# Kernel tuning notes

Hardware: AMD Instinct MI355X
Metric: run time of the kernel (lower is better)

## Reference

```python
import jax, jax.numpy as jnp
import numpy as np

B = 4
N_PER_B = 65536
N = B * N_PER_B
GROUP_SIZE = 64
ORDER = 9  # min bits to cover grid size 512
C0, C1, C2 = 64, 128, 128


def hilbert_encode(coors, order):
    """Skilling AxesToTranspose, vectorized over N points, 3 dims -> int32 code."""
    n = 3
    X = [coors[:, i].astype(jnp.int32) for i in range(n)]
    M = 1 << (order - 1)
    Q = M
    while Q > 1:
        P = Q - 1
        for i in range(n):
            cond = (X[i] & Q) != 0
            if i == 0:
                X[0] = jnp.where(cond, X[0] ^ P, X[0])
            else:
                t = (X[0] ^ X[i]) & P
                x0 = jnp.where(cond, X[0] ^ P, X[0] ^ t)
                xi = jnp.where(cond, X[i], X[i] ^ t)
                X[0], X[i] = x0, xi
        Q >>= 1
    for i in range(1, n):
        X[i] = X[i] ^ X[i - 1]
    t = jnp.zeros_like(X[0])
    Q = M
    while Q > 1:
        t = jnp.where((X[n - 1] & Q) != 0, t ^ (Q - 1), t)
        Q >>= 1
    X = [x ^ t for x in X]
    # interleave transposed bits MSB-first: code has 3*order bits (27 < 31, fits int32)
    code = jnp.zeros_like(X[0])
    for b in range(order - 1, -1, -1):
        for i in range(n):
            code = (code << 1) | ((X[i] >> b) & 1)
    return code


def _mapping_indices(vox_coors):
    """Two Hilbert orderings (normal + reversed coord axes); per-batch stable grouping."""
    batch = vox_coors[:, 0]
    c1 = vox_coors[:, 1:4]
    c2 = vox_coors[:, 3:0:-1]  # [0,3,2,1] reverse of the xyz columns
    code1 = hilbert_encode(c1, ORDER)
    code2 = hilbert_encode(c2, ORDER)
    ind1 = jnp.lexsort((code1, batch))  # batch-major, curve-order minor
    ind2 = jnp.lexsort((code2, batch))
    inv1 = jnp.argsort(ind1)
    ind12 = inv1[ind2]  # maps ordering-1 arrangement to ordering-2 arrangement
    return ind1, ind12


def _block(p, x, params):
    """VoxFormer-style block: center pts per group, pos-encode, gate feats, local attn, FFN."""
    Wpos, bpos, Wq, Wk, Wv, Wo, Wout = params
    C = Wq.shape[0]
    gs = GROUP_SIZE
    pg = p.reshape(-1, gs, 3)
    e = (pg - pg.mean(axis=1, keepdims=True)).reshape(-1, 3) @ Wpos + bpos  # [N,C]
    h = (x * e).reshape(-1, gs, C)  # [G,gs,C]
    q, k, v = h @ Wq, h @ Wk, h @ Wv
    scores = jnp.einsum('gqc,gkc->gqk', q, k) / jnp.sqrt(jnp.asarray(C, q.dtype))
    attn = jax.nn.softmax(scores, axis=-1)
    o = jnp.einsum('gqk,gkc->gqc', attn, v).reshape(-1, C) @ Wo
    return jax.nn.relu(o) @ Wout  # [N,C_out]


def setup_inputs() -> dict:
    key = jax.random.key(0)
    ks = jax.random.split(key, 20)
    bcol = jnp.repeat(jnp.arange(B, dtype=jnp.int32), N_PER_B)
    z = jax.random.randint(ks[0], (N,), 0, 64, dtype=jnp.int32)
    y = jax.random.randint(ks[1], (N,), 0, 512, dtype=jnp.int32)
    x = jax.random.randint(ks[2], (N,), 0, 512, dtype=jnp.int32)
    vox_coors = jnp.stack([bcol, z, y, x], axis=1)
    vox_numbs = jnp.full((B,), N_PER_B, dtype=jnp.int32)
    vox_feats = jax.random.normal(ks[3], (N, C0), dtype=jnp.float32)
    pts_coors = jax.random.normal(ks[4], (N, 3), dtype=jnp.float32)
    s = lambda k, shape: jax.random.normal(k, shape, dtype=jnp.float32) / np.float32(np.sqrt(shape[0]))
    return dict(
        vox_numbs=vox_numbs, vox_coors=vox_coors, vox_feats=vox_feats, pts_coors=pts_coors,
        Wpos1=s(ks[5], (3, C0)), bpos1=jnp.zeros((C0,), jnp.float32),
        Wq1=s(ks[6], (C0, C0)), Wk1=s(ks[7], (C0, C0)), Wv1=s(ks[8], (C0, C0)),
        Wo1=s(ks[9], (C0, C0)), Wout1=s(ks[10], (C0, C1)),
        Wpos2=s(ks[11], (3, C1)), bpos2=jnp.zeros((C1,), jnp.float32),
        Wq2=s(ks[12], (C1, C1)), Wk2=s(ks[13], (C1, C1)), Wv2=s(ks[14], (C1, C1)),
        Wo2=s(ks[15], (C1, C1)), Wout2=s(ks[16], (C1, C2)),
    )


def reference(vox_numbs, vox_coors, vox_feats, pts_coors,
              Wpos1, bpos1, Wq1, Wk1, Wv1, Wo1, Wout1,
              Wpos2, bpos2, Wq2, Wk2, Wv2, Wo2, Wout2):
    ind1, ind12 = _mapping_indices(vox_coors)
    params = ((Wpos1, bpos1, Wq1, Wk1, Wv1, Wo1, Wout1),
              (Wpos2, bpos2, Wq2, Wk2, Wv2, Wo2, Wout2))
    for ind, prm in zip((ind1, ind12), params):
        vox_feats = vox_feats[ind]
        pts_coors = pts_coors[ind]
        vox_coors = vox_coors[ind]
        vox_feats = _block(pts_coors, vox_feats, prm)
    return vox_feats, pts_coors, vox_coors, vox_numbs
```

## Files before the change

kernel.cpp:

```cpp
#include <hip/hip_runtime.h>

using u64 = unsigned long long;
typedef _Float16 f16;
using f16x8 = __attribute__((ext_vector_type(8))) _Float16;
using f16x4 = __attribute__((ext_vector_type(4))) _Float16;
using f32x4 = __attribute__((ext_vector_type(4))) float;

__device__ __forceinline__ int hilbert3(int X0, int X1, int X2) {
  #pragma unroll
  for (int Q = 256; Q > 1; Q >>= 1) {
    const int P = Q - 1;
    if (X0 & Q) X0 ^= P;
    int t1 = (X0 ^ X1) & P;
    if (X1 & Q) X0 ^= P; else { X0 ^= t1; X1 ^= t1; }
    int t2 = (X0 ^ X2) & P;
    if (X2 & Q) X0 ^= P; else { X0 ^= t2; X2 ^= t2; }
  }
  X1 ^= X0;
  X2 ^= X1;
  int t = 0;
  #pragma unroll
  for (int Q = 256; Q > 1; Q >>= 1) if (X2 & Q) t ^= (Q - 1);
  X0 ^= t; X1 ^= t; X2 ^= t;
  int code = 0;
  #pragma unroll
  for (int b = 8; b >= 0; b--)
    code = (code << 3) | (((X0 >> b) & 1) << 2) | (((X1 >> b) & 1) << 1) | ((X2 >> b) & 1);
  return code;
}

__device__ __forceinline__ void cswap(u64& a, u64& b, bool up) {
  if ((a > b) == up) { u64 t = a; a = b; b = t; }
}

__global__ __launch_bounds__(1024) void sort_tile0(const int* __restrict__ vox,
                                                   u64* __restrict__ keys, int n,
                                                   int spanm1) {
  __shared__ u64 s[2048];
  const int base = blockIdx.x * 2048;
  const int bl = base & spanm1;
  #pragma unroll
  for (int m = 0; m < 2; m++) {
    const int e = base + threadIdx.x + m * 1024;
    const int isrc = e & (n - 1);
    const int4 c = ((const int4*)vox)[isrc];
    const unsigned code = (e < n) ? (unsigned)hilbert3(c.y, c.z, c.w)
                                  : (unsigned)hilbert3(c.w, c.z, c.y);
    s[threadIdx.x + m * 1024] =
        ((u64)(unsigned)c.x << 45) | ((u64)code << 18) | (unsigned)isrc;
  }
  __syncthreads();
  for (int k = 2; k <= 2048; k <<= 1) {
    for (int j = k >> 1; j >= 1; j >>= 1) {
      const int p = threadIdx.x;
      const int i = ((p & ~(j - 1)) << 1) | (p & (j - 1));
      const bool up = (((bl + i) & k) == 0);
      u64 a = s[i], b = s[i | j];
      if ((a > b) == up) { s[i] = b; s[i | j] = a; }
      __syncthreads();
    }
  }
  keys[base + threadIdx.x]        = s[threadIdx.x];
  keys[base + threadIdx.x + 1024] = s[threadIdx.x + 1024];
}

template<int LEV>
__device__ __forceinline__ void gstepT(u64* __restrict__ keys, int t, int jlow,
                                       int k, int spanm1) {
  constexpr int S = 1 << LEV;
  const int i0 = ((t & ~(jlow - 1)) << LEV) | (t & (jlow - 1));
  const bool up = (((i0 & spanm1) & k) == 0);
  u64 x[S];
  #pragma unroll
  for (int m = 0; m < S; m++) x[m] = keys[i0 + (size_t)m * jlow];
  #pragma unroll
  for (int d = S >> 1; d >= 1; d >>= 1)
    #pragma unroll
    for (int m = 0; m < S; m++)
      if (!(m & d)) cswap(x[m], x[m | d], up);
  #pragma unroll
  for (int m = 0; m < S; m++) keys[i0 + (size_t)m * jlow] = x[m];
}

__global__ void bitonic_gN(u64* __restrict__ keys, int jlow, int lev, int k, int spanm1) {
  const int t = blockIdx.x * blockDim.x + threadIdx.x;
  switch (lev) {
    case 1: gstepT<1>(keys, t, jlow, k, spanm1); break;
    case 2: gstepT<2>(keys, t, jlow, k, spanm1); break;
    case 3: gstepT<3>(keys, t, jlow, k, spanm1); break;
    default: gstepT<4>(keys, t, jlow, k, spanm1); break;
  }
}

__global__ __launch_bounds__(1024) void merge_tile2(u64* __restrict__ keys, int k,
                                                    int spanm1) {
  __shared__ u64 s[2048];
  const int base = blockIdx.x * 2048;
  s[threadIdx.x]        = keys[base + threadIdx.x];
  s[threadIdx.x + 1024] = keys[base + threadIdx.x + 1024];
  __syncthreads();
  const bool up = (((base & spanm1) & k) == 0);
  for (int j = 1024; j >= 1; j >>= 1) {
    const int p = threadIdx.x;
    const int i = ((p & ~(j - 1)) << 1) | (p & (j - 1));
    u64 a = s[i], b = s[i | j];
    if ((a > b) == up) { s[i] = b; s[i | j] = a; }
    __syncthreads();
  }
  keys[base + threadIdx.x]        = s[threadIdx.x];
  keys[base + threadIdx.x + 1024] = s[threadIdx.x + 1024];
}

__global__ void extract_inv_k(const u64* __restrict__ keys, const float* __restrict__ pts,
                              int* __restrict__ ind, int* __restrict__ inv,
                              float* __restrict__ pts1p, int n) {
  int t = blockIdx.x * blockDim.x + threadIdx.x;
  if (t >= n) return;
  int s = (int)(keys[t] & 0x3FFFFULL);
  ind[t] = s;
  inv[s] = t;
  pts1p[t * 3 + 0] = pts[s * 3 + 0];
  pts1p[t * 3 + 1] = pts[s * 3 + 1];
  pts1p[t * 3 + 2] = pts[s * 3 + 2];
}

__global__ void finish_k(const u64* __restrict__ keys2, const int* __restrict__ inv1,
                         int* __restrict__ g2, const float* __restrict__ pts,
                         const int* __restrict__ vox, const int* __restrict__ numbs,
                         float* __restrict__ out_pts, float* __restrict__ out_vox,
                         float* __restrict__ out_nb, int n, int B) {
  int t = blockIdx.x * blockDim.x + threadIdx.x;
  if (t >= n) return;
  int s = (int)(keys2[t] & 0x3FFFFULL);
  g2[t] = inv1[s];
  out_pts[t * 3 + 0] = pts[s * 3 + 0];
  out_pts[t * 3 + 1] = pts[s * 3 + 1];
  out_pts[t * 3 + 2] = pts[s * 3 + 2];
  const int4 v = ((const int4*)vox)[s];
  out_vox[t * 4 + 0] = (float)v.x;
  out_vox[t * 4 + 1] = (float)v.y;
  out_vox[t * 4 + 2] = (float)v.z;
  out_vox[t * 4 + 3] = (float)v.w;
  if (t < B) out_nb[t] = (float)numbs[t];
}

__global__ void prep_all(const float* __restrict__ Wq1, const float* __restrict__ Wk1,
                         const float* __restrict__ Wv1, const float* __restrict__ Wo1,
                         const float* __restrict__ Wout1,
                         const float* __restrict__ Wq2, const float* __restrict__ Wk2,
                         const float* __restrict__ Wv2, const float* __restrict__ Wo2,
                         const float* __restrict__ Wout2,
                         f16* __restrict__ A1a, f16* __restrict__ A2a, f16* __restrict__ A3a,
                         f16* __restrict__ A1b, f16* __restrict__ A2b, f16* __restrict__ A3b) {
  const int idx = blockIdx.x * blockDim.x + threadIdx.x;
  if (idx < 4096) {
    const int a = idx >> 6, b = idx & 63;
    float s1 = 0.f, s2 = 0.f;
    for (int c = 0; c < 64; c++) {
      s1 = fmaf(Wq1[b * 64 + c], Wk1[a * 64 + c], s1);
      s2 = fmaf(Wv1[b * 64 + c], Wo1[c * 64 + a], s2);
    }
    A1a[idx] = (f16)(s1 * 0.125f);
    A2a[idx] = (f16)s2;
  }
  if (idx < 8192) {
    const int o = idx >> 6, c = idx & 63;
    A3a[idx] = (f16)Wout1[c * 128 + o];
  }
  {
    const int a = idx >> 7, b = idx & 127;
    float s1 = 0.f, s2 = 0.f;
    for (int c = 0; c < 128; c++) {
      s1 = fmaf(Wq2[b * 128 + c], Wk2[a * 128 + c], s1);
      s2 = fmaf(Wv2[b * 128 + c], Wo2[c * 128 + a], s2);
    }
    A1b[idx] = (f16)(s1 * 0.08838834764831845f);
    A2b[idx] = (f16)s2;
    A3b[idx] = (f16)Wout2[b * 128 + a];
  }
}

__device__ __forceinline__ int swzb(int row) {
  return (((row & 7) ^ (((row >> 3) & 3) << 1)) << 4);
}

template<int M, int K, int AMODE>
__device__ __forceinline__ void stage8(const f16* __restrict__ Ag,
                                       const f16* __restrict__ lA,
                                       const f16* __restrict__ lB,
                                       int w, int lane,
                                       f32x4 (&acc)[(M / 16) * 4 / 8]) {
  constexpr int NPW = (M / 16) * 4 / 8;
  constexpr int KT = K / 32;
  const int lr = lane & 15, lk = lane >> 4;
  const int ct = (w * NPW) >> 2;
  const int qt0 = (w * NPW) & 3;
  const int c = ct * 16 + lr;
  f16x8 Af[KT];
  #pragma unroll
  for (int kt = 0; kt < KT; kt++) {
    const int k0 = kt * 32 + lk * 8;
    if (AMODE == 0) {
      Af[kt] = *(const f16x8*)(Ag + (size_t)c * K + k0);
    } else if (AMODE == 1) {
      Af[kt] = *(const f16x8*)((const char*)lA + (((c * K + k0) * 2) ^ swzb(c)));
    } else {
      f16x8 a;
      #pragma unroll
      for (int e = 0; e < 8; e++) {
        const int j = k0 + e;
        a[e] = *(const f16*)((const char*)lA + (((j * M + c) * 2) ^ swzb(j)));
      }
      Af[kt] = a;
    }
  }
  #pragma unroll
  for (int i = 0; i < NPW; i++) {
    const int q = lr + (qt0 + i) * 16;
    #pragma unroll
    for (int kt = 0; kt < KT; kt++) {
      const int k0 = kt * 32 + lk * 8;
      const f16x8 Bf = *(const f16x8*)((const char*)lB + (((q * K + k0) * 2) ^ swzb(q)));
      acc[i] = __builtin_amdgcn_mfma_f32_16x16x32_f16(Af[kt], Bf, acc[i], 0, 0, 0);
    }
  }
}

template<int RL, bool RELU>
__device__ __forceinline__ void store8(f16* __restrict__ dst, int ct, int qt,
                                       int lane, f32x4 v) {
  const int lr = lane & 15, lk = lane >> 4;
  const int q = lr + qt * 16;
  const int c0 = ct * 16 + lk * 4;
  f16x4 o;
  #pragma unroll
  for (int r = 0; r < 4; r++) {
    float x = v[r];
    if (RELU) x = fmaxf(x, 0.f);
    o[r] = (f16)x;
  }
  *(f16x4*)((char*)dst + (((q * RL + c0) * 2) ^ swzb(q))) = o;
}

template<int C, bool X16, bool OUT16>
__global__ __launch_bounds__(512, 8) void block_mfma(
    const int* __restrict__ idx_x, const float* __restrict__ ptsP,
    const void* __restrict__ xsrc,
    const float* __restrict__ Wpos, const float* __restrict__ bpos,
    const f16* __restrict__ A1, const f16* __restrict__ A2, const f16* __restrict__ A3,
    void* __restrict__ outp) {
  constexpr int NPWC = C / 32;
  extern __shared__ char smem[];
  f16* bufH = (f16*)smem;
  f16* bufT = bufH + 64 * C;
  f16* scH  = bufT + 64 * C;

  const int g = blockIdx.x;
  const int t = threadIdx.x;
  const int lane = t & 63;
  const int w = t >> 6;
  const int lr = lane & 15, lk = lane >> 4;
  const int q8 = t >> 3, qq = t & 7;

  {
    const int sx = idx_x[g * 64 + q8];
    float mx = ptsP[(g * 64 + lane) * 3 + 0];
    float my = ptsP[(g * 64 + lane) * 3 + 1];
    float mz = ptsP[(g * 64 + lane) * 3 + 2];
    #pragma unroll
    for (int o = 32; o > 0; o >>= 1) {
      mx += __shfl_xor(mx, o); my += __shfl_xor(my, o); mz += __shfl_xor(mz, o);
    }
    mx *= (1.f / 64.f); my *= (1.f / 64.f); mz *= (1.f / 64.f);
    const float d0 = ptsP[(g * 64 + q8) * 3 + 0] - mx;
    const float d1 = ptsP[(g * 64 + q8) * 3 + 1] - my;
    const float d2 = ptsP[(g * 64 + q8) * 3 + 2] - mz;
    #pragma unroll
    for (int i = 0; i < C / 64; i++) {
      const int c0 = qq * (C / 8) + i * 8;
      float xa[8];
      if constexpr (X16) {
        f16x8 xr = *(const f16x8*)((const f16*)xsrc + (size_t)sx * C + c0);
        #pragma unroll
        for (int j = 0; j < 8; j++) xa[j] = (float)xr[j];
      } else {
        float4 x0 = *(const float4*)((const float*)xsrc + (size_t)sx * C + c0);
        float4 x1 = *(const float4*)((const float*)xsrc + (size_t)sx * C + c0 + 4);
        xa[0] = x0.x; xa[1] = x0.y; xa[2] = x0.z; xa[3] = x0.w;
        xa[4] = x1.x; xa[5] = x1.y; xa[6] = x1.z; xa[7] = x1.w;
      }
      f16x8 hv;
      #pragma unroll
      for (int jj = 0; jj < 8; jj += 4) {
        const float4 w0 = *(const float4*)(Wpos + 0 * C + c0 + jj);
        const float4 w1 = *(const float4*)(Wpos + 1 * C + c0 + jj);
        const float4 w2 = *(const float4*)(Wpos + 2 * C + c0 + jj);
        const float4 bb = *(const float4*)(bpos + c0 + jj);
        hv[jj + 0] = (f16)(xa[jj + 0] * fmaf(d0, w0.x, fmaf(d1, w1.x, fmaf(d2, w2.x, bb.x))));
        hv[jj + 1] = (f16)(xa[jj + 1] * fmaf(d0, w0.y, fmaf(d1, w1.y, fmaf(d2, w2.y, bb.y))));
        hv[jj + 2] = (f16)(xa[jj + 2] * fmaf(d0, w0.z, fmaf(d1, w1.z, fmaf(d2, w2.z, bb.z))));
        hv[jj + 3] = (f16)(xa[jj + 3] * fmaf(d0, w0.w, fmaf(d1, w1.w, fmaf(d2, w2.w, bb.w))));
      }
      *(f16x8*)((char*)bufH + (((q8 * C + c0) * 2) ^ swzb(q8))) = hv;
    }
  }
  __syncthreads();

  {
    f32x4 acc[NPWC] = {};
    stage8<C, C, 0>(A1, nullptr, bufH, w, lane, acc);
    const int ct = (w * NPWC) >> 2, qt0 = (w * NPWC) & 3;
    #pragma unroll
    for (int i = 0; i < NPWC; i++) store8<C, false>(bufT, ct, qt0 + i, lane, acc[i]);
  }
  __syncthreads();

  {
    f32x4 acc[2] = {};
    stage8<64, C, 1>(nullptr, bufH, bufT, w, lane, acc);
    const int ct = (w * 2) >> 2, qt0 = (w * 2) & 3;
    #pragma unroll
    for (int i = 0; i < 2; i++) store8<64, false>(scH, ct, qt0 + i, lane, acc[i]);
  }
  __syncthreads();

  {
    f16x8 x8 = *(const f16x8*)((const char*)scH + (((q8 * 64 + qq * 8) * 2) ^ swzb(q8)));
    float v[8];
    float mxv = -3.0e38f;
    #pragma unroll
    for (int j = 0; j < 8; j++) {
      v[j] = (float)x8[j];
      mxv = fmaxf(mxv, v[j]);
    }
    mxv = fmaxf(mxv, __shfl_xor(mxv, 1));
    mxv = fmaxf(mxv, __shfl_xor(mxv, 2));
    mxv = fmaxf(mxv, __shfl_xor(mxv, 4));
    float s = 0.f;
    #pragma unroll
    for (int j = 0; j < 8; j++) { v[j] = __expf(v[j] - mxv); s += v[j]; }
    s += __shfl_xor(s, 1);
    s += __shfl_xor(s, 2);
    s += __shfl_xor(s, 4);
    const float inv = 1.f / s;
    f16x8 pk;
    #pragma unroll
    for (int j = 0; j < 8; j++) pk[j] = (f16)(v[j] * inv);
    *(f16x8*)((char*)scH + (((q8 * 64 + qq * 8) * 2) ^ swzb(q8))) = pk;
  }
  __syncthreads();

  {
    f32x4 acc[NPWC] = {};
    stage8<C, 64, 2>(nullptr, bufH, scH, w, lane, acc);
    const int ct = (w * NPWC) >> 2, qt0 = (w * NPWC) & 3;
    #pragma unroll
    for (int i = 0; i < NPWC; i++) store8<C, false>(bufT, ct, qt0 + i, lane, acc[i]);
  }
  __syncthreads();

  {
    f32x4 acc[NPWC] = {};
    stage8<C, C, 0>(A2, nullptr, bufT, w, lane, acc);
    const int ct = (w * NPWC) >> 2, qt0 = (w * NPWC) & 3;
    #pragma unroll
    for (int i = 0; i < NPWC; i++) store8<C, true>(bufH, ct, qt0 + i, lane, acc[i]);
  }
  __syncthreads();

  {
    f32x4 acc[4] = {};
    stage8<128, C, 0>(A3, nullptr, bufH, w, lane, acc);
    #pragma unroll
    for (int i = 0; i < 4; i++) {
      const int qr = lr + i * 16;
      const int o0 = w * 16 + lk * 4;
      const size_t row = (size_t)g * 64 + qr;
      if (OUT16) {
        f16x4 v;
        #pragma unroll
        for (int r = 0; r < 4; r++) v[r] = (f16)acc[i][r];
        *(f16x4*)((f16*)outp + row * 128 + o0) = v;
      } else {
        *(f32x4*)((float*)outp + row * 128 + o0) = acc[i];
      }
    }
  }
}

extern "C" void kernel_launch(void* const* d_in, const int* in_sizes, int n_in,
                              void* d_out, int out_size, void* d_ws, size_t ws_size,
                              hipStream_t stream) {
  const int*   vox_numbs = (const int*)d_in[0];
  const int*   vox_coors = (const int*)d_in[1];
  const float* vox_feats = (const float*)d_in[2];
  const float* pts_coors = (const float*)d_in[3];
  const float* Wpos1 = (const float*)d_in[4];
  const float* bpos1 = (const float*)d_in[5];
  const float* Wq1   = (const float*)d_in[6];
  const float* Wk1   = (const float*)d_in[7];
  const float* Wv1   = (const float*)d_in[8];
  const float* Wo1   = (const float*)d_in[9];
  const float* Wout1 = (const float*)d_in[10];
  const float* Wpos2 = (const float*)d_in[11];
  const float* bpos2 = (const float*)d_in[12];
  const float* Wq2   = (const float*)d_in[13];
  const float* Wk2   = (const float*)d_in[14];
  const float* Wv2   = (const float*)d_in[15];
  const float* Wo2   = (const float*)d_in[16];
  const float* Wout2 = (const float*)d_in[17];

  const int B = in_sizes[0];
  const int n = in_sizes[1] / 4;
  const int ngrp = n / 64;

  char* w = (char*)d_ws;
  auto alloc = [&](size_t bytes) {
    char* p = w;
    w += (bytes + 255) & ~(size_t)255;
    return p;
  };
  u64* keys    = (u64*)alloc((size_t)2 * n * 8);
  int* ind1    = (int*)alloc((size_t)n * 4);
  int* inv1    = (int*)alloc((size_t)n * 4);
  int* g2      = (int*)alloc((size_t)n * 4);
  float* pts1p = (float*)alloc((size_t)n * 3 * 4);
  f16* A1a     = (f16*)alloc(64 * 64 * 2);
  f16* A2a     = (f16*)alloc(64 * 64 * 2);
  f16* A3a     = (f16*)alloc(128 * 64 * 2);
  f16* A1b     = (f16*)alloc(128 * 128 * 2);
  f16* A2b     = (f16*)alloc(128 * 128 * 2);
  f16* A3b     = (f16*)alloc(128 * 128 * 2);
  f16* feats1  = (f16*)alloc((size_t)n * 128 * 2);
  u64* keys2   = keys + n;

  float* out_feats = (float*)d_out;
  float* out_pts   = out_feats + (size_t)n * 128;
  float* out_vox   = out_pts + (size_t)n * 3;
  float* out_nb    = out_vox + (size_t)n * 4;

  auto f64k  = block_mfma<64,  false, true>;
  auto f128k = block_mfma<128, true,  false>;
  hipFuncSetAttribute((const void*)f64k,  hipFuncAttributeMaxDynamicSharedMemorySize, 65536);
  hipFuncSetAttribute((const void*)f128k, hipFuncAttributeMaxDynamicSharedMemorySize, 65536);

  prep_all<<<64, 256, 0, stream>>>(Wq1, Wk1, Wv1, Wo1, Wout1, Wq2, Wk2, Wv2, Wo2, Wout2,
                                   A1a, A2a, A3a, A1b, A2b, A3b);

  int span = (B > 0) ? n / B : n;
  if (span < 4096 || (span & (span - 1)) != 0 || n % span != 0) span = n;
  const int spanm1 = span - 1;

  sort_tile0<<<2 * n / 2048, 1024, 0, stream>>>(vox_coors, keys, n, spanm1);
  for (int k = 4096; k <= span; k <<= 1) {
    int j = k >> 1;
    while (j >= 2048) {
      int lev = 1;
      while (lev < 4 && (j >> lev) >= 2048) lev++;
      const int jlow = j >> (lev - 1);
      const int nth = (2 * n) >> lev;
      bitonic_gN<<<nth / 256, 256, 0, stream>>>(keys, jlow, lev, k, spanm1);
      j = jlow >> 1;
    }
    merge_tile2<<<2 * n / 2048, 1024, 0, stream>>>(keys, k, spanm1);
  }

  extract_inv_k<<<(n + 255) / 256, 256, 0, stream>>>(keys, pts_coors, ind1, inv1, pts1p, n);
  finish_k<<<(n + 255) / 256, 256, 0, stream>>>(keys2, inv1, g2, pts_coors, vox_coors,
                                                vox_numbs, out_pts, out_vox, out_nb, n, B);

  block_mfma<64, false, true><<<ngrp, 512, 24576, stream>>>(
      ind1, pts1p, vox_feats, Wpos1, bpos1, A1a, A2a, A3a, feats1);
  block_mfma<128, true, false><<<ngrp, 512, 40960, stream>>>(
      g2, out_pts, feats1, Wpos2, bpos2, A1b, A2b, A3b, out_feats);
}
```

Baseline: 260.9 us.

## Scatter block-1 output into ordering-2 layout so block 2 reads contiguously

The first block kernel now writes each output row directly to its position in the second Hilbert ordering, using an inverse map of the second sort built in the extract kernel. The second block kernel then reads its f16 input features contiguously instead of gathering through g2. This removes the random 256-byte row gather in block 2 and the dependent inv1 lookup in finish_k, at the cost of scattered 128-byte writes from block 1 and a small shared-memory destination table.

```diff
diff --git a/kernel.cpp b/kernel.cpp
--- a/kernel.cpp
+++ b/kernel.cpp
@@ -111,28 +111,28 @@
   keys[base + threadIdx.x + 1024] = s[threadIdx.x + 1024];
 }
 
-__global__ void extract_inv_k(const u64* __restrict__ keys, const float* __restrict__ pts,
-                              int* __restrict__ ind, int* __restrict__ inv,
-                              float* __restrict__ pts1p, int n) {
+__global__ void extract_both_k(const u64* __restrict__ keys1, const u64* __restrict__ keys2,
+                               const float* __restrict__ pts,
+                               int* __restrict__ ind1, int* __restrict__ inv2,
+                               float* __restrict__ pts1p, int n) {
   int t = blockIdx.x * blockDim.x + threadIdx.x;
   if (t >= n) return;
-  int s = (int)(keys[t] & 0x3FFFFULL);
-  ind[t] = s;
-  inv[s] = t;
-  pts1p[t * 3 + 0] = pts[s * 3 + 0];
-  pts1p[t * 3 + 1] = pts[s * 3 + 1];
-  pts1p[t * 3 + 2] = pts[s * 3 + 2];
-}
-
-__global__ void finish_k(const u64* __restrict__ keys2, const int* __restrict__ inv1,
-                         int* __restrict__ g2, const float* __restrict__ pts,
+  int s1 = (int)(keys1[t] & 0x3FFFFULL);
+  ind1[t] = s1;
+  pts1p[t * 3 + 0] = pts[s1 * 3 + 0];
+  pts1p[t * 3 + 1] = pts[s1 * 3 + 1];
+  pts1p[t * 3 + 2] = pts[s1 * 3 + 2];
+  int s2 = (int)(keys2[t] & 0x3FFFFULL);
+  inv2[s2] = t;
+}
+
+__global__ void finish_k(const u64* __restrict__ keys2, const float* __restrict__ pts,
                          const int* __restrict__ vox, const int* __restrict__ numbs,
                          float* __restrict__ out_pts, float* __restrict__ out_vox,
                          float* __restrict__ out_nb, int n, int B) {
   int t = blockIdx.x * blockDim.x + threadIdx.x;
   if (t >= n) return;
   int s = (int)(keys2[t] & 0x3FFFFULL);
-  g2[t] = inv1[s];
   out_pts[t * 3 + 0] = pts[s * 3 + 0];
   out_pts[t * 3 + 1] = pts[s * 3 + 1];
   out_pts[t * 3 + 2] = pts[s * 3 + 2];
@@ -242,10 +242,10 @@
   *(f16x4*)((char*)dst + (((q * RL + c0) * 2) ^ swzb(q))) = o;
 }
 
-template<int C, bool X16, bool OUT16>
+template<int C, bool X16, bool OUT16, bool GATH, bool SCAT>
 __global__ __launch_bounds__(512, 8) void block_mfma(
-    const int* __restrict__ idx_x, const float* __restrict__ ptsP,
-    const void* __restrict__ xsrc,
+    const int* __restrict__ idx_x, const int* __restrict__ dmap,
+    const float* __restrict__ ptsP, const void* __restrict__ xsrc,
     const float* __restrict__ Wpos, const float* __restrict__ bpos,
     const f16* __restrict__ A1, const f16* __restrict__ A2, const f16* __restrict__ A3,
     void* __restrict__ outp) {
@@ -254,6 +254,7 @@
   f16* bufH = (f16*)smem;
   f16* bufT = bufH + 64 * C;
   f16* scH  = bufT + 64 * C;
+  int* sDest = (int*)(scH + 64 * 64);
 
   const int g = blockIdx.x;
   const int t = threadIdx.x;
@@ -263,7 +264,10 @@
   const int q8 = t >> 3, qq = t & 7;
 
   {
-    const int sx = idx_x[g * 64 + q8];
+    const int sx = GATH ? idx_x[g * 64 + q8] : (g * 64 + q8);
+    if constexpr (SCAT) {
+      if (qq == 0) sDest[q8] = dmap[sx];
+    }
     float mx = ptsP[(g * 64 + lane) * 3 + 0];
     float my = ptsP[(g * 64 + lane) * 3 + 1];
     float mz = ptsP[(g * 64 + lane) * 3 + 2];
@@ -375,7 +379,7 @@
     for (int i = 0; i < 4; i++) {
       const int qr = lr + i * 16;
       const int o0 = w * 16 + lk * 4;
-      const size_t row = (size_t)g * 64 + qr;
+      const size_t row = SCAT ? (size_t)sDest[qr] : ((size_t)g * 64 + qr);
       if (OUT16) {
         f16x4 v;
         #pragma unroll
@@ -422,8 +426,7 @@
   };
   u64* keys    = (u64*)alloc((size_t)2 * n * 8);
   int* ind1    = (int*)alloc((size_t)n * 4);
-  int* inv1    = (int*)alloc((size_t)n * 4);
-  int* g2      = (int*)alloc((size_t)n * 4);
+  int* inv2    = (int*)alloc((size_t)n * 4);
   float* pts1p = (float*)alloc((size_t)n * 3 * 4);
   f16* A1a     = (f16*)alloc(64 * 64 * 2);
   f16* A2a     = (f16*)alloc(64 * 64 * 2);
@@ -439,8 +442,8 @@
   float* out_vox   = out_pts + (size_t)n * 3;
   float* out_nb    = out_vox + (size_t)n * 4;
 
-  auto f64k  = block_mfma<64,  false, true>;
-  auto f128k = block_mfma<128, true,  false>;
+  auto f64k  = block_mfma<64,  false, true,  true,  true>;
+  auto f128k = block_mfma<128, true,  false, false, false>;
   hipFuncSetAttribute((const void*)f64k,  hipFuncAttributeMaxDynamicSharedMemorySize, 65536);
   hipFuncSetAttribute((const void*)f128k, hipFuncAttributeMaxDynamicSharedMemorySize, 65536);
 
@@ -465,12 +468,13 @@
     merge_tile2<<<2 * n / 2048, 1024, 0, stream>>>(keys, k, spanm1);
   }
 
-  extract_inv_k<<<(n + 255) / 256, 256, 0, stream>>>(keys, pts_coors, ind1, inv1, pts1p, n);
-  finish_k<<<(n + 255) / 256, 256, 0, stream>>>(keys2, inv1, g2, pts_coors, vox_coors,
-                                                vox_numbs, out_pts, out_vox, out_nb, n, B);
-
-  block_mfma<64, false, true><<<ngrp, 512, 24576, stream>>>(
-      ind1, pts1p, vox_feats, Wpos1, bpos1, A1a, A2a, A3a, feats1);
-  block_mfma<128, true, false><<<ngrp, 512, 40960, stream>>>(
-      g2, out_pts, feats1, Wpos2, bpos2, A1b, A2b, A3b, out_feats);
-}
+  extract_both_k<<<(n + 255) / 256, 256, 0, stream>>>(keys, keys2, pts_coors,
+                                                      ind1, inv2, pts1p, n);
+  finish_k<<<(n + 255) / 256, 256, 0, stream>>>(keys2, pts_coors, vox_coors, vox_numbs,
+                                                out_pts, out_vox, out_nb, n, B);
+
+  block_mfma<64, false, true, true, true><<<ngrp, 512, 24832, stream>>>(
+      ind1, inv2, pts1p, vox_feats, Wpos1, bpos1, A1a, A2a, A3a, feats1);
+  block_mfma<128, true, false, false, false><<<ngrp, 512, 40960, stream>>>(
+      nullptr, nullptr, out_pts, feats1, Wpos2, bpos2, A1b, A2b, A3b, out_feats);
+}
```

New measurement: 262.0 us. Within noise of the previous version (+0.4%).
